# Kernel optimization log

Measured on AMD Instinct MI355X. Metric: run time of the kernel, lower is better.

The kernel has to match this reference:

```python
import jax, jax.numpy as jnp
import numpy as np

NX = 1024
N_HEAD = 16
HEAD_DIM = NX // N_HEAD
RPE_MAX = 20
LN_EPS = 1e-5


def _layernorm(h, g, b, eps=LN_EPS):
    mu = jnp.mean(h, axis=-1, keepdims=True)
    var = jnp.var(h, axis=-1, keepdims=True)
    return (h - mu) * jax.lax.rsqrt(var + eps) * g + b


def setup_inputs() -> dict:
    key = jax.random.key(0)
    ks = jax.random.split(key, 12)
    B, S = 2, 1024
    x = jax.random.normal(ks[0], (B, S, NX), dtype=jnp.float32)
    local_info = jax.random.normal(ks[1], (B, S, NX), dtype=jnp.float32)
    attention_mask = jnp.zeros((B, 1, 1, S), dtype=jnp.float32)
    pairwise_dist = jax.random.randint(ks[2], (B, S, S), -RPE_MAX, RPE_MAX + 1, dtype=jnp.int32)
    s = 0.02
    Wqkv = jax.random.normal(ks[3], (NX, 3 * NX), dtype=jnp.float32) * s
    bqkv = jnp.zeros((3 * NX,), dtype=jnp.float32)
    Wproj = jax.random.normal(ks[4], (NX, NX), dtype=jnp.float32) * s
    bproj = jnp.zeros((NX,), dtype=jnp.float32)
    rpek = jax.random.normal(ks[5], (2 * RPE_MAX + 1, HEAD_DIM), dtype=jnp.float32) * s
    ln1_g = jnp.ones((NX,), dtype=jnp.float32)
    ln1_b = jnp.zeros((NX,), dtype=jnp.float32)
    gate_W = jax.random.normal(ks[6], (2 * NX, NX), dtype=jnp.float32) * s
    return {"x": x, "local_info": local_info, "attention_mask": attention_mask,
            "pairwise_dist": pairwise_dist, "Wqkv": Wqkv, "bqkv": bqkv,
            "Wproj": Wproj, "bproj": bproj, "rpek": rpek,
            "ln1_g": ln1_g, "ln1_b": ln1_b, "gate_W": gate_W}


def reference(x, local_info, attention_mask, pairwise_dist, Wqkv, bqkv, Wproj, bproj, rpek, ln1_g, ln1_b, gate_W):
    B, S, _ = x.shape
    qkv = x @ Wqkv + bqkv                      # [B,S,3*NX]
    q, k, v = jnp.split(qkv, 3, axis=-1)
    q = q.reshape(B, S, N_HEAD, HEAD_DIM)
    k = k.reshape(B, S, N_HEAD, HEAD_DIM)
    v = v.reshape(B, S, N_HEAD, HEAD_DIM)
    # content scores [B,H,Q,K]
    w = jnp.einsum('bqhd,bkhd->bhqk', q, k)
    # relative-position bias: embedding lookup + per-query matmul
    k_rpe = rpek[pairwise_dist + RPE_MAX]      # [B,Q,K,D]
    w_rpe = jnp.einsum('bqhd,bqkd->bhqk', q, k_rpe)
    w = (w + w_rpe) / jnp.float32(HEAD_DIM) ** 0.5
    w = w + attention_mask
    p = jax.nn.softmax(w, axis=-1)
    a = jnp.einsum('bhqk,bkhd->bqhd', p, v).reshape(B, S, NX)
    a = a @ Wproj + bproj
    # residual + LN1
    h = _layernorm(x + a, ln1_g, ln1_b)
    # gated fusion of local and global info
    z = jax.nn.sigmoid(jnp.concatenate([local_info, h], axis=-1) @ gate_W)
    out = (1.0 - z) * h + z * local_info
    return out
```

## Files before the change

### kernel.cpp

```cpp
#include <hip/hip_runtime.h>
#include <hip/hip_bf16.h>

#define SEQ 1024
#define NH 16
#define HD 64
#define NXD 1024

typedef unsigned short u16;
typedef unsigned char u8;
typedef __attribute__((ext_vector_type(8))) short short8;
typedef __attribute__((ext_vector_type(4))) float f32x4;

__device__ __forceinline__ u16 f2bf(float f) {
    __hip_bfloat16 h = __float2bfloat16(f);
    u16 u; __builtin_memcpy(&u, &h, 2); return u;
}
__device__ __forceinline__ float bf2f(u16 u) {
    __hip_bfloat16 h; __builtin_memcpy(&h, &u, 2); return __bfloat162float(h);
}

__device__ __forceinline__ void gld16(const void* g, void* l) {
    __builtin_amdgcn_global_load_lds(
        (const __attribute__((address_space(1))) void*)g,
        (__attribute__((address_space(3))) void*)l, 16, 0, 0);
}

__device__ __forceinline__ void transpose_tile(const float* __restrict__ src,
        u16* __restrict__ dst, int R, int C, int bx, int by) {
    __shared__ float tile[32][33];
    int r0 = by * 32, c0 = bx * 32;
    int tr = threadIdx.x >> 3, tc = (threadIdx.x & 7) * 4;
    float4 v = *(const float4*)(src + (size_t)(r0 + tr) * C + c0 + tc);
    tile[tr][tc+0] = v.x; tile[tr][tc+1] = v.y; tile[tr][tc+2] = v.z; tile[tr][tc+3] = v.w;
    __syncthreads();
    u16* d = dst + (size_t)(c0 + tr) * R + r0 + tc;
    #pragma unroll
    for (int j = 0; j < 4; j++) d[j] = f2bf(tile[tc+j][tr]);
}

__global__ __launch_bounds__(256) void prep_all(const float* __restrict__ x,
        const float* __restrict__ local, const int* __restrict__ pd,
        const float* __restrict__ Wqkv, const float* __restrict__ Wproj,
        const float* __restrict__ gateW,
        u16* __restrict__ xb, u16* __restrict__ gateA, u8* __restrict__ pdu8,
        u16* __restrict__ WqkvT, u16* __restrict__ WprojT, u16* __restrict__ gateWT) {
    int bid = blockIdx.x;
    if (bid < 2048) {
        int i = (bid * 256 + threadIdx.x) * 4;
        float4 v = *(const float4*)(x + i);
        xb[i+0] = f2bf(v.x); xb[i+1] = f2bf(v.y); xb[i+2] = f2bf(v.z); xb[i+3] = f2bf(v.w);
    } else if (bid < 4096) {
        int i = ((bid - 2048) * 256 + threadIdx.x) * 4;
        int row = i >> 10, c = i & 1023;
        float4 v = *(const float4*)(local + i);
        u16* d = gateA + (size_t)row * 2048 + c;
        d[0] = f2bf(v.x); d[1] = f2bf(v.y); d[2] = f2bf(v.z); d[3] = f2bf(v.w);
    } else if (bid < 6144) {
        int i = ((bid - 4096) * 256 + threadIdx.x) * 4;
        int4 v = *(const int4*)(pd + i);
        uchar4 o;
        o.x = (u8)(v.x + 20); o.y = (u8)(v.y + 20);
        o.z = (u8)(v.z + 20); o.w = (u8)(v.w + 20);
        *(uchar4*)(pdu8 + i) = o;
    } else if (bid < 9216) {
        int k = bid - 6144;  transpose_tile(Wqkv,  WqkvT,  1024, 3072, k % 96, k / 96);
    } else if (bid < 10240) {
        int k = bid - 9216;  transpose_tile(Wproj, WprojT, 1024, 1024, k % 32, k / 32);
    } else {
        int k = bid - 10240; transpose_tile(gateW, gateWT, 2048, 1024, k % 32, k / 32);
    }
}

__global__ __launch_bounds__(256) void trq_kernel(const u16* __restrict__ vb,
        u16* __restrict__ vTb, const u16* __restrict__ qb,
        const float* __restrict__ rpek, u16* __restrict__ qrpe16) {
    int bid = blockIdx.x;
    if (bid < 2048) {
        __shared__ u16 tile[32][33];
        int bh = bid >> 6, d0 = ((bid >> 5) & 1) * 32, s0 = (bid & 31) * 32;
        int tr = threadIdx.x >> 3, tc = (threadIdx.x & 7) * 4;
        const u16* s = vb + ((size_t)bh * SEQ + s0 + tr) * HD + d0 + tc;
        #pragma unroll
        for (int j = 0; j < 4; j++) tile[tr][tc+j] = s[j];
        __syncthreads();
        u16* d = vTb + ((size_t)bh * HD + d0 + tr) * SEQ + s0 + tc;
        #pragma unroll
        for (int j = 0; j < 4; j++) d[j] = tile[tc+j][tr];
    } else {
        int t = threadIdx.x, lane = t & 63, wid = t >> 6;
        int quad = lane >> 4, l16 = lane & 15;
        int r0 = ((bid - 2048) * 4 + wid) * 16;
        short8 af[2];
        #pragma unroll
        for (int s = 0; s < 2; s++)
            af[s] = *(const short8*)(qb + (size_t)(r0 + l16) * HD + s * 32 + quad * 8);
        #pragma unroll
        for (int nt = 0; nt < 3; nt++) {
            int n = nt * 16 + l16;
            const float* rp = rpek + (size_t)(n < 41 ? n : 40) * HD;
            f32x4 acc = {0.f, 0.f, 0.f, 0.f};
            #pragma unroll
            for (int s = 0; s < 2; s++) {
                float4 f0 = *(const float4*)(rp + s * 32 + quad * 8);
                float4 f1 = *(const float4*)(rp + s * 32 + quad * 8 + 4);
                short8 bf;
                bf[0] = (short)f2bf(f0.x); bf[1] = (short)f2bf(f0.y);
                bf[2] = (short)f2bf(f0.z); bf[3] = (short)f2bf(f0.w);
                bf[4] = (short)f2bf(f1.x); bf[5] = (short)f2bf(f1.y);
                bf[6] = (short)f2bf(f1.z); bf[7] = (short)f2bf(f1.w);
                acc = __builtin_amdgcn_mfma_f32_16x16x32_bf16(af[s], bf, acc, 0, 0, 0);
            }
            if (n < 41) {
                #pragma unroll
                for (int r = 0; r < 4; r++)
                    qrpe16[(size_t)(r0 + quad * 4 + r) * 48 + n] = f2bf(acc[r]);
            }
        }
    }
}

template<int BM, int BN, int EPI>
__global__ __launch_bounds__(256) void gemm_bt(
        const u16* __restrict__ A, int lda, const u16* __restrict__ BT, int K,
        const float* __restrict__ bias, float* __restrict__ out_f,
        u16* __restrict__ oq, u16* __restrict__ ok, u16* __restrict__ ov,
        const u16* __restrict__ h16, const float* __restrict__ loc32,
        float* __restrict__ outg) {
    const int LOGBM = (BM == 128) ? 7 : 6;
    const int LOGBN = (BN == 128) ? 7 : 6;
    const int MT = BM / 32, NT = BN / 32;
    __shared__ u16 Al[8 * BM * 8];
    __shared__ u16 Bl[8 * BN * 8];
    int t = threadIdx.x, lane = t & 63, wid = t >> 6;
    int quad = lane >> 4, l16 = lane & 15;
    int m0 = blockIdx.y * BM, n0 = blockIdx.x * BN;
    int waveM = wid >> 1, waveN = wid & 1;
    f32x4 acc[MT][NT] = {};
    for (int k0 = 0; k0 < K; k0 += 64) {
        __syncthreads();
        #pragma unroll
        for (int i = 0; i < BM / 32; i++) {
            int c = t + i * 256, c0 = c & ~63;
            int m = c & (BM - 1), kb = c >> LOGBM;
            gld16(A + (size_t)(m0 + m) * lda + k0 + kb * 8,
                  &Al[((c0 >> LOGBM) * BM + (c0 & (BM - 1))) * 8]);
        }
        #pragma unroll
        for (int i = 0; i < BN / 32; i++) {
            int c = t + i * 256, c0 = c & ~63;
            int n = c & (BN - 1), kb = c >> LOGBN;
            gld16(BT + (size_t)(n0 + n) * K + k0 + kb * 8,
                  &Bl[((c0 >> LOGBN) * BN + (c0 & (BN - 1))) * 8]);
        }
        __syncthreads();
        short8 af[MT][2], bfr[NT][2];
        #pragma unroll
        for (int s = 0; s < 2; s++) {
            #pragma unroll
            for (int mt = 0; mt < MT; mt++)
                af[mt][s] = *(short8*)&Al[((s * 4 + quad) * BM + waveM * (BM / 2) + mt * 16 + l16) * 8];
            #pragma unroll
            for (int nt = 0; nt < NT; nt++)
                bfr[nt][s] = *(short8*)&Bl[((s * 4 + quad) * BN + waveN * (BN / 2) + nt * 16 + l16) * 8];
        }
        #pragma unroll
        for (int mt = 0; mt < MT; mt++)
            #pragma unroll
            for (int nt = 0; nt < NT; nt++) {
                acc[mt][nt] = __builtin_amdgcn_mfma_f32_16x16x32_bf16(af[mt][0], bfr[nt][0], acc[mt][nt], 0, 0, 0);
                acc[mt][nt] = __builtin_amdgcn_mfma_f32_16x16x32_bf16(af[mt][1], bfr[nt][1], acc[mt][nt], 0, 0, 0);
            }
    }
    #pragma unroll
    for (int mt = 0; mt < MT; mt++)
        #pragma unroll
        for (int nt = 0; nt < NT; nt++)
            #pragma unroll
            for (int r = 0; r < 4; r++) {
                int row = m0 + waveM * (BM / 2) + mt * 16 + quad * 4 + r;
                int col = n0 + waveN * (BN / 2) + nt * 16 + l16;
                float val = acc[mt][nt][r];
                if (EPI == 0) {
                    val += bias[col];
                    int b = row >> 10, s = row & 1023;
                    int sec = col >> 10, cc = col & 1023;
                    int h = cc >> 6, d = cc & 63;
                    u16 bv = f2bf(val);
                    size_t qidx = (((size_t)(b * NH + h)) * SEQ + s) * HD + d;
                    if (sec == 0)      oq[qidx] = bv;
                    else if (sec == 1) ok[qidx] = bv;
                    else               ov[qidx] = bv;
                } else if (EPI == 1) {
                    out_f[(size_t)row * 1024 + col] = val + bias[col];
                } else {
                    float z = 1.f / (1.f + __expf(-val));
                    size_t idx = (size_t)row * 1024 + col;
                    float hv = bf2f(h16[(size_t)row * 2048 + 1024 + col]);
                    outg[idx] = (1.f - z) * hv + z * loc32[idx];
                }
            }
}

__global__ __launch_bounds__(256) void attn_kernel(
        const u16* __restrict__ qb, const u16* __restrict__ kmat,
        const u16* __restrict__ vTb, const u16* __restrict__ qrpe16,
        const u8* __restrict__ pdu8, const float* __restrict__ mask,
        u16* __restrict__ po0, u16* __restrict__ po1, float* __restrict__ pl) {
    __shared__ u16 Kl[8 * 64 * 8];
    __shared__ u16 Vl[8 * 64 * 8];
    __shared__ u16 Pl[4][8 * 16 * 8];
    __shared__ u16 qr_lds[64 * 48];
    __shared__ u8 pdl[64 * 80];
    int t = threadIdx.x, lane = t & 63, wid = t >> 6;
    int quad = lane >> 4, l16 = lane & 15;

    int id = blockIdx.x;
    int xcd = id & 7, j = id >> 3;
    int b = xcd >> 2;
    int head = ((xcd & 3) << 2) | (j >> 5);
    int qblk = ((j >> 1) & 15) << 6;
    int sp = j & 1;
    int bh = (b << 4) | head;
    int q0 = qblk + wid * 16;

    {
        const u16* src = qrpe16 + ((size_t)bh * SEQ + qblk) * 48;
        { int c = t, c0 = c & ~63; gld16(src + (size_t)c * 8, &qr_lds[c0 * 8]); }
        if (wid < 2) { int c = 256 + t, c0 = c & ~63; gld16(src + (size_t)c * 8, &qr_lds[c0 * 8]); }
    }

    short8 aq[2];
    #pragma unroll
    for (int s = 0; s < 2; s++)
        aq[s] = *(const short8*)(qb + ((size_t)bh * SEQ + q0 + l16) * HD + s * 32 + quad * 8);
    f32x4 o[4] = {};
    float lrow[4] = {0.f, 0.f, 0.f, 0.f};
    u16* Pw = Pl[wid];
    const u8* pdbase = pdu8 + ((size_t)b * SEQ + qblk) * SEQ;
    for (int kt = 0; kt < 8; kt++) {
        int k0 = sp * 512 + kt * 64;
        __syncthreads();
        #pragma unroll
        for (int i = 0; i < 2; i++) {
            int c = t + i * 256, c0 = c & ~63;
            int s = c & 63, g = c >> 6, g0 = c0 >> 6;
            gld16(kmat + ((size_t)bh * SEQ + k0 + s) * HD + g * 8, &Kl[(g0 * 64) * 8]);
            gld16(vTb + ((size_t)bh * HD + s) * SEQ + k0 + g * 8, &Vl[(g0 * 64) * 8]);
        }
        {
            int qrow = t >> 2, kj = (t & 3) * 16;
            uint4 pv = *(const uint4*)(pdbase + (size_t)qrow * SEQ + k0 + kj);
            *(uint4*)&pdl[qrow * 80 + kj] = pv;
        }
        __syncthreads();
        #pragma unroll
        for (int ks = 0; ks < 4; ks++) {
            f32x4 a = {0.f, 0.f, 0.f, 0.f};
            #pragma unroll
            for (int dh = 0; dh < 2; dh++) {
                short8 bk = *(short8*)&Kl[((dh * 4 + quad) * 64 + ks * 16 + l16) * 8];
                a = __builtin_amdgcn_mfma_f32_16x16x32_bf16(aq[dh], bk, a, 0, 0, 0);
            }
            int kcol = k0 + ks * 16 + l16;
            float mk = mask[b * SEQ + kcol];
            int kcl = ks * 16 + l16;
            #pragma unroll
            for (int r = 0; r < 4; r++) {
                int ql = wid * 16 + quad * 4 + r;
                int pdv = pdl[ql * 80 + kcl];
                float rpe = bf2f(qr_lds[ql * 48 + pdv]);
                float sc = (a[r] + rpe) * 0.125f + mk;
                float p = __expf(fminf(sc, 30.f));
                lrow[r] += p;
                Pw[((kcl >> 3) * 16 + quad * 4 + r) * 8 + (kcl & 7)] = f2bf(p);
            }
        }
        asm volatile("s_waitcnt lgkmcnt(0)" ::: "memory");
        #pragma unroll
        for (int ks2 = 0; ks2 < 2; ks2++) {
            short8 pa = *(short8*)&Pw[((ks2 * 4 + quad) * 16 + l16) * 8];
            #pragma unroll
            for (int dt = 0; dt < 4; dt++) {
                short8 vv = *(short8*)&Vl[((ks2 * 4 + quad) * 64 + dt * 16 + l16) * 8];
                o[dt] = __builtin_amdgcn_mfma_f32_16x16x32_bf16(pa, vv, o[dt], 0, 0, 0);
            }
        }
    }
    #pragma unroll
    for (int r = 0; r < 4; r++) {
        #pragma unroll
        for (int off = 1; off < 16; off <<= 1)
            lrow[r] += __shfl_xor(lrow[r], off, 16);
    }
    u16* po = sp ? po1 : po0;
    #pragma unroll
    for (int r = 0; r < 4; r++) {
        int row = bh * SEQ + q0 + quad * 4 + r;
        #pragma unroll
        for (int dt = 0; dt < 4; dt++)
            po[(size_t)row * 64 + dt * 16 + l16] = f2bf(o[dt][r]);
        if (l16 == 0)
            pl[sp * 32768 + row] = lrow[r];
    }
}

__global__ __launch_bounds__(256) void attn_combine(const u16* __restrict__ po0,
        const u16* __restrict__ po1, const float* __restrict__ pl,
        u16* __restrict__ aoutb) {
    int idx = blockIdx.x * 256 + threadIdx.x;
    int row = idx >> 6, d = idx & 63;
    float l0 = pl[row], l1 = pl[32768 + row];
    float inv = 1.f / (l0 + l1);
    float o0 = bf2f(po0[(size_t)row * 64 + d]);
    float o1 = bf2f(po1[(size_t)row * 64 + d]);
    float val = (o0 + o1) * inv;
    int bh = row >> 10, qrow = row & 1023;
    int b = bh >> 4, h = bh & 15;
    aoutb[((size_t)(b * SEQ + qrow)) * NXD + h * HD + d] = f2bf(val);
}

__device__ __forceinline__ float block_sum(float v, float* sred) {
    #pragma unroll
    for (int o = 32; o > 0; o >>= 1) v += __shfl_down(v, o, 64);
    int lane = threadIdx.x & 63, wid = threadIdx.x >> 6;
    __syncthreads();
    if (lane == 0) sred[wid] = v;
    __syncthreads();
    return sred[0] + sred[1] + sred[2] + sred[3];
}

__global__ __launch_bounds__(256) void ln_kernel(const float* __restrict__ x,
        const float* __restrict__ a, const float* __restrict__ g,
        const float* __restrict__ bln, u16* __restrict__ gateA) {
    int row = blockIdx.x;
    __shared__ float sred[4];
    float vals[4];
    float s = 0.f;
    #pragma unroll
    for (int i = 0; i < 4; i++) {
        int c = threadIdx.x + i * 256;
        vals[i] = x[(size_t)row * NXD + c] + a[(size_t)row * NXD + c];
        s += vals[i];
    }
    s = block_sum(s, sred);
    float mu = s * (1.f / NXD);
    float vs = 0.f;
    #pragma unroll
    for (int i = 0; i < 4; i++) { float d = vals[i] - mu; vs += d * d; }
    vs = block_sum(vs, sred);
    float rstd = rsqrtf(vs * (1.f / NXD) + 1e-5f);
    #pragma unroll
    for (int i = 0; i < 4; i++) {
        int c = threadIdx.x + i * 256;
        float hv = (vals[i] - mu) * rstd * g[c] + bln[c];
        gateA[(size_t)row * 2048 + 1024 + c] = f2bf(hv);
    }
}

extern "C" void kernel_launch(void* const* d_in, const int* in_sizes, int n_in,
                              void* d_out, int out_size, void* d_ws, size_t ws_size,
                              hipStream_t stream) {
    const float* x     = (const float*)d_in[0];
    const float* local = (const float*)d_in[1];
    const float* mask  = (const float*)d_in[2];
    const int*   pd    = (const int*)d_in[3];
    const float* Wqkv  = (const float*)d_in[4];
    const float* bqkv  = (const float*)d_in[5];
    const float* Wproj = (const float*)d_in[6];
    const float* bproj = (const float*)d_in[7];
    const float* rpek  = (const float*)d_in[8];
    const float* ln_g  = (const float*)d_in[9];
    const float* ln_b  = (const float*)d_in[10];
    const float* gateW = (const float*)d_in[11];
    float* out = (float*)d_out;

    char* ws = (char*)d_ws;
    const size_t MB = 1u << 20;
    u16*   xb    = (u16*)(ws + 0);
    u16*   WqkvT = (u16*)(ws + 4 * MB);
    u16*   po0   = (u16*)(ws + 4 * MB);
    float* pl    = (float*)(ws + 8 * MB);
    u16*   WprojT= (u16*)(ws + 10 * MB);
    u16*   qb    = (u16*)(ws + 12 * MB);
    u16*   kb    = (u16*)(ws + 16 * MB);
    u16*   vb    = (u16*)(ws + 20 * MB);
    u16*   po1   = (u16*)(ws + 20 * MB);
    float* pout  = (float*)(ws + 16 * MB);
    u16*   vTb   = (u16*)(ws + 24 * MB);
    u16*   qrpe16= (u16*)(ws + 28 * MB);
    u16*   gateA = (u16*)(ws + 34 * MB);
    u8*    pdu8  = (u8*)(ws + 42 * MB);
    u16*   gateWT= (u16*)(ws + 44 * MB);
    u16*   aoutb = xb;

    prep_all<<<12288, 256, 0, stream>>>(x, local, pd, Wqkv, Wproj, gateW,
            xb, gateA, pdu8, WqkvT, WprojT, gateWT);
    gemm_bt<128, 128, 0><<<dim3(24, 16), 256, 0, stream>>>(xb, 1024, WqkvT, 1024, bqkv,
            nullptr, qb, kb, vb, nullptr, nullptr, nullptr);
    trq_kernel<<<2560, 256, 0, stream>>>(vb, vTb, qb, rpek, qrpe16);
    attn_kernel<<<1024, 256, 0, stream>>>(qb, kb, vTb, qrpe16, pdu8, mask,
            po0, po1, pl);
    attn_combine<<<8192, 256, 0, stream>>>(po0, po1, pl, aoutb);
    gemm_bt<64, 64, 1><<<dim3(16, 32), 256, 0, stream>>>(aoutb, 1024, WprojT, 1024, bproj,
            pout, nullptr, nullptr, nullptr, nullptr, nullptr, nullptr);
    ln_kernel<<<2048, 256, 0, stream>>>(x, pout, ln_g, ln_b, gateA);
    gemm_bt<64, 64, 2><<<dim3(16, 32), 256, 0, stream>>>(gateA, 2048, gateWT, 2048, nullptr,
            nullptr, nullptr, nullptr, nullptr, gateA, local, out);
}
```

Measured before the change: 258.3 us.

## Double-buffer GEMM LDS tiles with async prefetch and shrink QKV tile width

```diff
diff --git a/kernel.cpp b/kernel.cpp
--- a/kernel.cpp
+++ b/kernel.cpp
@@ -23,6 +23,13 @@
     __builtin_amdgcn_global_load_lds(
         (const __attribute__((address_space(1))) void*)g,
         (__attribute__((address_space(3))) void*)l, 16, 0, 0);
+}
+
+template<int N> __device__ __forceinline__ void waitcnt_vm() {
+    asm volatile("s_waitcnt vmcnt(%0)" :: "n"(N) : "memory");
+}
+__device__ __forceinline__ void raw_barrier() {
+    asm volatile("s_barrier" ::: "memory");
 }
 
 __device__ __forceinline__ void transpose_tile(const float* __restrict__ src,
@@ -129,39 +136,55 @@
     const int LOGBM = (BM == 128) ? 7 : 6;
     const int LOGBN = (BN == 128) ? 7 : 6;
     const int MT = BM / 32, NT = BN / 32;
-    __shared__ u16 Al[8 * BM * 8];
-    __shared__ u16 Bl[8 * BN * 8];
+    const int LPT = BM / 32 + BN / 32;
+    __shared__ u16 Al[2][8 * BM * 8];
+    __shared__ u16 Bl[2][8 * BN * 8];
     int t = threadIdx.x, lane = t & 63, wid = t >> 6;
     int quad = lane >> 4, l16 = lane & 15;
     int m0 = blockIdx.y * BM, n0 = blockIdx.x * BN;
     int waveM = wid >> 1, waveN = wid & 1;
     f32x4 acc[MT][NT] = {};
-    for (int k0 = 0; k0 < K; k0 += 64) {
-        __syncthreads();
+
+    auto stage = [&](int buf, int k0) {
         #pragma unroll
         for (int i = 0; i < BM / 32; i++) {
             int c = t + i * 256, c0 = c & ~63;
             int m = c & (BM - 1), kb = c >> LOGBM;
             gld16(A + (size_t)(m0 + m) * lda + k0 + kb * 8,
-                  &Al[((c0 >> LOGBM) * BM + (c0 & (BM - 1))) * 8]);
+                  &Al[buf][((c0 >> LOGBM) * BM + (c0 & (BM - 1))) * 8]);
         }
         #pragma unroll
         for (int i = 0; i < BN / 32; i++) {
             int c = t + i * 256, c0 = c & ~63;
             int n = c & (BN - 1), kb = c >> LOGBN;
             gld16(BT + (size_t)(n0 + n) * K + k0 + kb * 8,
-                  &Bl[((c0 >> LOGBN) * BN + (c0 & (BN - 1))) * 8]);
-        }
-        __syncthreads();
+                  &Bl[buf][((c0 >> LOGBN) * BN + (c0 & (BN - 1))) * 8]);
+        }
+    };
+
+    const int NTILES = K >> 6;
+    stage(0, 0);
+    for (int tt = 0; tt < NTILES; tt++) {
+        int cur = tt & 1;
+        raw_barrier();
+        if (tt + 1 < NTILES) {
+            stage(cur ^ 1, (tt + 1) << 6);
+            waitcnt_vm<LPT>();
+        } else {
+            waitcnt_vm<0>();
+        }
+        raw_barrier();
+        const u16* Ac = Al[cur];
+        const u16* Bc = Bl[cur];
         short8 af[MT][2], bfr[NT][2];
         #pragma unroll
         for (int s = 0; s < 2; s++) {
             #pragma unroll
             for (int mt = 0; mt < MT; mt++)
-                af[mt][s] = *(short8*)&Al[((s * 4 + quad) * BM + waveM * (BM / 2) + mt * 16 + l16) * 8];
+                af[mt][s] = *(const short8*)&Ac[((s * 4 + quad) * BM + waveM * (BM / 2) + mt * 16 + l16) * 8];
             #pragma unroll
             for (int nt = 0; nt < NT; nt++)
-                bfr[nt][s] = *(short8*)&Bl[((s * 4 + quad) * BN + waveN * (BN / 2) + nt * 16 + l16) * 8];
+                bfr[nt][s] = *(const short8*)&Bc[((s * 4 + quad) * BN + waveN * (BN / 2) + nt * 16 + l16) * 8];
         }
         #pragma unroll
         for (int mt = 0; mt < MT; mt++)
@@ -395,7 +418,7 @@
 
     prep_all<<<12288, 256, 0, stream>>>(x, local, pd, Wqkv, Wproj, gateW,
             xb, gateA, pdu8, WqkvT, WprojT, gateWT);
-    gemm_bt<128, 128, 0><<<dim3(24, 16), 256, 0, stream>>>(xb, 1024, WqkvT, 1024, bqkv,
+    gemm_bt<128, 64, 0><<<dim3(48, 16), 256, 0, stream>>>(xb, 1024, WqkvT, 1024, bqkv,
             nullptr, qb, kb, vb, nullptr, nullptr, nullptr);
     trq_kernel<<<2560, 256, 0, stream>>>(vb, vTb, qb, rpek, qrpe16);
     attn_kernel<<<1024, 256, 0, stream>>>(qb, kb, vTb, qrpe16, pdu8, mask,
```

Measured after the change: 258.6 us. About the same (+0.1%).

## Load GEMM fragments directly from global with register double-buffering and XCD-aware block swizzle

Applied to the files above, without the earlier changes.

```diff
diff --git a/kernel.cpp b/kernel.cpp
--- a/kernel.cpp
+++ b/kernel.cpp
@@ -119,58 +119,59 @@
     }
 }
 
-template<int BM, int BN, int EPI>
+template<int BM, int BN, int EPI, int KTOT, int LDA, int CHX, int CHY>
 __global__ __launch_bounds__(256) void gemm_bt(
-        const u16* __restrict__ A, int lda, const u16* __restrict__ BT, int K,
+        const u16* __restrict__ A, const u16* __restrict__ BT,
         const float* __restrict__ bias, float* __restrict__ out_f,
         u16* __restrict__ oq, u16* __restrict__ ok, u16* __restrict__ ov,
         const u16* __restrict__ h16, const float* __restrict__ loc32,
         float* __restrict__ outg) {
-    const int LOGBM = (BM == 128) ? 7 : 6;
-    const int LOGBN = (BN == 128) ? 7 : 6;
     const int MT = BM / 32, NT = BN / 32;
-    __shared__ u16 Al[8 * BM * 8];
-    __shared__ u16 Bl[8 * BN * 8];
     int t = threadIdx.x, lane = t & 63, wid = t >> 6;
     int quad = lane >> 4, l16 = lane & 15;
-    int m0 = blockIdx.y * BM, n0 = blockIdx.x * BN;
+    int id = blockIdx.x + (CHX * 4) * blockIdx.y;
+    int xcd = id & 7, li = id >> 3;
+    int bxs = (xcd & 3) * CHX + li % CHX;
+    int bys = (xcd >> 2) * CHY + li / CHX;
+    int m0 = bys * BM, n0 = bxs * BN;
     int waveM = wid >> 1, waveN = wid & 1;
+    const u16* Abase = A + (size_t)(m0 + waveM * (BM / 2) + l16) * LDA;
+    const u16* Bbase = BT + (size_t)(n0 + waveN * (BN / 2) + l16) * KTOT;
     f32x4 acc[MT][NT] = {};
-    for (int k0 = 0; k0 < K; k0 += 64) {
-        __syncthreads();
-        #pragma unroll
-        for (int i = 0; i < BM / 32; i++) {
-            int c = t + i * 256, c0 = c & ~63;
-            int m = c & (BM - 1), kb = c >> LOGBM;
-            gld16(A + (size_t)(m0 + m) * lda + k0 + kb * 8,
-                  &Al[((c0 >> LOGBM) * BM + (c0 & (BM - 1))) * 8]);
-        }
-        #pragma unroll
-        for (int i = 0; i < BN / 32; i++) {
-            int c = t + i * 256, c0 = c & ~63;
-            int n = c & (BN - 1), kb = c >> LOGBN;
-            gld16(BT + (size_t)(n0 + n) * K + k0 + kb * 8,
-                  &Bl[((c0 >> LOGBN) * BN + (c0 & (BN - 1))) * 8]);
-        }
-        __syncthreads();
-        short8 af[MT][2], bfr[NT][2];
+    short8 a0[MT][2], b0[NT][2], a1[MT][2], b1[NT][2];
+
+    auto LD = [&](short8 (&af)[MT][2], short8 (&bf)[NT][2], int k0) {
         #pragma unroll
         for (int s = 0; s < 2; s++) {
+            int ko = k0 + (s * 4 + quad) * 8;
             #pragma unroll
             for (int mt = 0; mt < MT; mt++)
-                af[mt][s] = *(short8*)&Al[((s * 4 + quad) * BM + waveM * (BM / 2) + mt * 16 + l16) * 8];
+                af[mt][s] = *(const short8*)(Abase + (size_t)mt * 16 * LDA + ko);
             #pragma unroll
             for (int nt = 0; nt < NT; nt++)
-                bfr[nt][s] = *(short8*)&Bl[((s * 4 + quad) * BN + waveN * (BN / 2) + nt * 16 + l16) * 8];
-        }
+                bf[nt][s] = *(const short8*)(Bbase + (size_t)nt * 16 * KTOT + ko);
+        }
+    };
+    auto MM = [&](short8 (&af)[MT][2], short8 (&bf)[NT][2]) {
         #pragma unroll
         for (int mt = 0; mt < MT; mt++)
             #pragma unroll
             for (int nt = 0; nt < NT; nt++) {
-                acc[mt][nt] = __builtin_amdgcn_mfma_f32_16x16x32_bf16(af[mt][0], bfr[nt][0], acc[mt][nt], 0, 0, 0);
-                acc[mt][nt] = __builtin_amdgcn_mfma_f32_16x16x32_bf16(af[mt][1], bfr[nt][1], acc[mt][nt], 0, 0, 0);
-            }
-    }
+                acc[mt][nt] = __builtin_amdgcn_mfma_f32_16x16x32_bf16(af[mt][0], bf[nt][0], acc[mt][nt], 0, 0, 0);
+                acc[mt][nt] = __builtin_amdgcn_mfma_f32_16x16x32_bf16(af[mt][1], bf[nt][1], acc[mt][nt], 0, 0, 0);
+            }
+    };
+
+    const int NTILES = KTOT >> 6;
+    LD(a0, b0, 0);
+    #pragma unroll
+    for (int tt = 0; tt < NTILES; tt += 2) {
+        LD(a1, b1, (tt + 1) << 6);
+        MM(a0, b0);
+        if (tt + 2 < NTILES) LD(a0, b0, (tt + 2) << 6);
+        MM(a1, b1);
+    }
+
     #pragma unroll
     for (int mt = 0; mt < MT; mt++)
         #pragma unroll
@@ -395,15 +396,15 @@
 
     prep_all<<<12288, 256, 0, stream>>>(x, local, pd, Wqkv, Wproj, gateW,
             xb, gateA, pdu8, WqkvT, WprojT, gateWT);
-    gemm_bt<128, 128, 0><<<dim3(24, 16), 256, 0, stream>>>(xb, 1024, WqkvT, 1024, bqkv,
-            nullptr, qb, kb, vb, nullptr, nullptr, nullptr);
+    gemm_bt<128, 64, 0, 1024, 1024, 12, 8><<<dim3(48, 16), 256, 0, stream>>>(
+            xb, WqkvT, bqkv, nullptr, qb, kb, vb, nullptr, nullptr, nullptr);
     trq_kernel<<<2560, 256, 0, stream>>>(vb, vTb, qb, rpek, qrpe16);
     attn_kernel<<<1024, 256, 0, stream>>>(qb, kb, vTb, qrpe16, pdu8, mask,
             po0, po1, pl);
     attn_combine<<<8192, 256, 0, stream>>>(po0, po1, pl, aoutb);
-    gemm_bt<64, 64, 1><<<dim3(16, 32), 256, 0, stream>>>(aoutb, 1024, WprojT, 1024, bproj,
-            pout, nullptr, nullptr, nullptr, nullptr, nullptr, nullptr);
+    gemm_bt<64, 64, 1, 1024, 1024, 4, 16><<<dim3(16, 32), 256, 0, stream>>>(
+            aoutb, WprojT, bproj, pout, nullptr, nullptr, nullptr, nullptr, nullptr, nullptr);
     ln_kernel<<<2048, 256, 0, stream>>>(x, pout, ln_g, ln_b, gateA);
-    gemm_bt<64, 64, 2><<<dim3(16, 32), 256, 0, stream>>>(gateA, 2048, gateWT, 2048, nullptr,
-            nullptr, nullptr, nullptr, nullptr, gateA, local, out);
-}
+    gemm_bt<64, 64, 2, 2048, 2048, 4, 16><<<dim3(16, 32), 256, 0, stream>>>(
+            gateA, gateWT, nullptr, nullptr, nullptr, nullptr, nullptr, gateA, local, out);
+}
```

After: 328.9 us. 27.3% more time.
